# Performance work log

Hardware: AMD Instinct MI355X
Metric: run time of the kernel (lower is better)

Reference implementation:

```python
import jax, jax.numpy as jnp
import numpy as np

H = 12        # query heads
KVH = 4       # key/value heads
D = 256       # head_dim = 3072 / 12
THETA = 1000042.0


def setup_inputs() -> dict:
    key = jax.random.key(0)
    ks = jax.random.split(key, 6)
    B, S, E = 1, 4096, 3072
    init = 0.02
    return {
        "hidden_states": jax.random.normal(ks[0], (B, S, E), jnp.float32),
        "attention_mask": jnp.ones((B, S), jnp.int32),
        "position_ids": jnp.arange(B * S, dtype=jnp.int32).reshape(B, S) % S,
        "Wq": jax.random.normal(ks[1], (E, H * D), jnp.float32) * init,
        "Wk": jax.random.normal(ks[2], (E, KVH * D), jnp.float32) * init,
        "Wv": jax.random.normal(ks[3], (E, KVH * D), jnp.float32) * init,
        "Wo": jax.random.normal(ks[4], (H * D, E), jnp.float32) * init,
    }


def _rotate_half(t):
    return jnp.concatenate([-t[..., D // 2:], t[..., : D // 2]], axis=-1)


def reference(hidden_states, attention_mask, position_ids, Wq, Wk, Wv, Wo):
    B, S, E = hidden_states.shape
    # QKV projections (no bias)
    q = (hidden_states @ Wq).reshape(B, S, H, D)
    k = (hidden_states @ Wk).reshape(B, S, KVH, D)
    v = (hidden_states @ Wv).reshape(B, S, KVH, D)
    # rotary embedding: sincos[pos] with half-split sin/cos, broadcast over heads
    inv_freq = jnp.asarray(1.0 / (THETA ** (np.arange(0, D, 2) / D)), jnp.float32)  # [D/2]
    freqs = position_ids.astype(jnp.float32)[..., None] * inv_freq                 # [B,S,D/2]
    emb = jnp.concatenate([freqs, freqs], axis=-1)[:, :, None, :]                  # [B,S,1,D]
    sin, cos = jnp.sin(emb), jnp.cos(emb)
    q = q * cos + _rotate_half(q) * sin
    k = k * cos + _rotate_half(k) * sin
    # GQA: repeat kv heads to match query heads
    kr = jnp.repeat(k, H // KVH, axis=2)  # [B,S,H,D]
    vr = jnp.repeat(v, H // KVH, axis=2)
    # causal mask combined with padding mask
    causal = jnp.tril(jnp.ones((S, S), bool))
    mask = (attention_mask > 0)[:, None, None, :] & causal[None, None]  # [B,1,S,S]
    neg = jnp.finfo(jnp.float32).min
    bias = jnp.where(mask, 0.0, neg).astype(jnp.float32)
    scores = jnp.einsum('bqhd,bkhd->bhqk', q, kr) / jnp.sqrt(jnp.float32(D)) + bias
    attn = jax.nn.softmax(scores, axis=-1)                 # [B,H,S,S]
    out = jnp.einsum('bhqk,bkhd->bqhd', attn, vr).reshape(B, S, H * D)
    return out @ Wo
```

## Files before the change

### kernel.cpp

```cpp
#include <hip/hip_runtime.h>
#include <hip/hip_bf16.h>
#include <math.h>
#include <stdint.h>

typedef unsigned short u16;
typedef __bf16 bf16x8 __attribute__((ext_vector_type(8)));
typedef float f32x4 __attribute__((ext_vector_type(4)));
typedef unsigned short u16x8 __attribute__((ext_vector_type(8)));
typedef unsigned short u16x4 __attribute__((ext_vector_type(4)));
typedef float f32x4v __attribute__((ext_vector_type(4)));

#define LOG2E 1.44269504088896340736f
#define S_LEN 4096
#define EMB 3072
#define NH 12
#define NKV 4
#define HD 256
#define KVDIM 1024

static __device__ __forceinline__ float b2f(u16 u) {
    union { unsigned int i; float f; } x; x.i = ((unsigned int)u) << 16; return x.f;
}
static __device__ __forceinline__ u16 f2b(float f) {
    union { float f; unsigned int i; } x; x.f = f;
    unsigned int r = (x.i + 0x7fffu + ((x.i >> 16) & 1u)) >> 16;
    return (u16)r;
}
static __device__ __forceinline__ f32x4 zero4() {
    f32x4 z; z[0] = 0.f; z[1] = 0.f; z[2] = 0.f; z[3] = 0.f; return z;
}
static __device__ __forceinline__ void gld_lds16(const void* g, void* l) {
    __builtin_amdgcn_global_load_lds(
        (__attribute__((address_space(1))) void*)(uintptr_t)g,
        (__attribute__((address_space(3))) void*)l, 16, 0, 0);
}

__global__ __launch_bounds__(256) void conv_f32_bf16(
    const float* __restrict__ in, u16* __restrict__ out, int n)
{
    int i = (blockIdx.x * 256 + threadIdx.x) * 4;
    if (i + 3 < n) {
        f32x4v v = *(const f32x4v*)(in + i);
        u16x4 o;
        o[0] = f2b(v[0]); o[1] = f2b(v[1]); o[2] = f2b(v[2]); o[3] = f2b(v[3]);
        *(u16x4*)(out + i) = o;
    } else {
        for (int j = i; j < n; ++j) out[j] = f2b(in[j]);
    }
}

__global__ __launch_bounds__(256) void transpose_f32_bf16(
    const float* __restrict__ in, u16* __restrict__ out, int R, int C)
{
    __shared__ u16 t[64][65];
    const int tid = threadIdx.x;
    const int c0 = blockIdx.x * 64, r0 = blockIdx.y * 64;
#pragma unroll
    for (int i = 0; i < 16; ++i) {
        int lin = i * 256 + tid;
        int r = lin >> 6, c = lin & 63;
        t[r][c] = f2b(in[(size_t)(r0 + r) * C + c0 + c]);
    }
    __syncthreads();
#pragma unroll
    for (int i = 0; i < 16; ++i) {
        int lin = i * 256 + tid;
        int c = lin >> 6, r = lin & 63;
        out[(size_t)(c0 + c) * R + r0 + r] = t[r][c];
    }
}

__global__ __launch_bounds__(256) void transpose_u16(
    const u16* __restrict__ in, u16* __restrict__ out, int R, int C)
{
    __shared__ u16 t[64][65];
    const int tid = threadIdx.x;
    const int c0 = blockIdx.x * 64, r0 = blockIdx.y * 64;
#pragma unroll
    for (int i = 0; i < 16; ++i) {
        int lin = i * 256 + tid;
        int r = lin >> 6, c = lin & 63;
        t[r][c] = in[(size_t)(r0 + r) * C + c0 + c];
    }
    __syncthreads();
#pragma unroll
    for (int i = 0; i < 16; ++i) {
        int lin = i * 256 + tid;
        int c = lin >> 6, r = lin & 63;
        out[(size_t)(c0 + c) * R + r0 + r] = t[r][c];
    }
}

__global__ __launch_bounds__(128) void sincos_kernel(
    const int* __restrict__ pos, float* __restrict__ tab)
{
    int s = blockIdx.x, t = threadIdx.x;
    float p = (float)pos[s];
    double e = (double)t / 128.0;
    float inv = (float)(1.0 / pow(1000042.0, e));
    float a = p * inv;
    tab[(size_t)s * 256 + t]       = cosf(a);
    tab[(size_t)s * 256 + 128 + t] = sinf(a);
}

__global__ __launch_bounds__(128) void rope_kernel(
    u16* __restrict__ Qb, u16* __restrict__ Kb, const float* __restrict__ tab)
{
    int s = blockIdx.x, hh = blockIdx.y, t = threadIdx.x;
    const float* cs = tab + (size_t)s * 256;
    float c = cs[t], sn = cs[128 + t];
    u16* row;
    float scale;
    if (hh < NH) { row = Qb + (size_t)s * EMB + hh * HD; scale = 0.0625f; }
    else         { row = Kb + (size_t)s * KVDIM + (size_t)(hh - NH) * HD; scale = 1.0f; }
    float a = b2f(row[t]), b = b2f(row[t + 128]);
    float oa = (a * c - b * sn) * scale;
    float ob = (b * c + a * sn) * scale;
    row[t] = f2b(oa); row[t + 128] = f2b(ob);
}

template <typename OutT>
__global__ __launch_bounds__(256) void gemm_bt(
    const u16* __restrict__ A, const u16* __restrict__ BT, OutT* __restrict__ C,
    int M, int N, int K)
{
    __shared__ __align__(16) u16 As[128 * 32];
    __shared__ __align__(16) u16 Bs[128 * 32];
    const int tid = threadIdx.x;
    const int lane = tid & 63, wid = tid >> 6;
    const int m0 = blockIdx.y * 128, n0 = blockIdx.x * 128;
    const int wm = (wid >> 1) * 64, wn = (wid & 1) * 64;
    const int g = lane >> 4, c16 = lane & 15;
    f32x4 acc[4][4];
#pragma unroll
    for (int i = 0; i < 4; ++i)
#pragma unroll
        for (int j = 0; j < 4; ++j) acc[i][j] = zero4();
    const int nk = K >> 5;
    const u16* Ab = A + (size_t)m0 * K;
    const u16* Bb = BT + (size_t)n0 * K;
    for (int kt = 0; kt < nk; ++kt) {
#pragma unroll
        for (int r2 = 0; r2 < 2; ++r2) {
            int chunk = r2 * 256 + tid;
            int row = chunk >> 2, c8 = chunk & 3;
            gld_lds16(Ab + (size_t)row * K + kt * 32 + c8 * 8, &As[chunk * 8]);
            gld_lds16(Bb + (size_t)row * K + kt * 32 + c8 * 8, &Bs[chunk * 8]);
        }
        __syncthreads();
        bf16x8 af[4], bfr[4];
#pragma unroll
        for (int i = 0; i < 4; ++i) {
            af[i]  = *(const bf16x8*)&As[(wm + i * 16 + c16) * 32 + g * 8];
            bfr[i] = *(const bf16x8*)&Bs[(wn + i * 16 + c16) * 32 + g * 8];
        }
#pragma unroll
        for (int i = 0; i < 4; ++i)
#pragma unroll
            for (int j = 0; j < 4; ++j)
                acc[i][j] = __builtin_amdgcn_mfma_f32_16x16x32_bf16(af[i], bfr[j], acc[i][j], 0, 0, 0);
        __syncthreads();
    }
#pragma unroll
    for (int i = 0; i < 4; ++i)
#pragma unroll
        for (int j = 0; j < 4; ++j)
#pragma unroll
            for (int r = 0; r < 4; ++r) {
                int row = m0 + wm + i * 16 + g * 4 + r;
                int col = n0 + wn + j * 16 + c16;
                if constexpr (sizeof(OutT) == 2)
                    C[(size_t)row * N + col] = f2b(acc[i][j][r]);
                else
                    C[(size_t)row * N + col] = acc[i][j][r];
            }
}

__global__ __launch_bounds__(256) void attn_kernel(
    u16* __restrict__ Q, const u16* __restrict__ Kb, const u16* __restrict__ VtG,
    const int* __restrict__ am)
{
    __shared__ __align__(16) u16 Ks[32 * 256];
    __shared__ __align__(16) u16 Vt[256 * 32];
    __shared__ __align__(16) u16 Ps[4][16 * 40];
    const int tid = threadIdx.x;
    const int lane = tid & 63, wid = tid >> 6;
    const int bx = blockIdx.x;
    const int qb = (S_LEN / 64 - 1) - (bx / NH);
    const int h  = bx % NH;
    const int kvh = h / 3;
    const int g = lane >> 4, c16 = lane & 15;

    bf16x8 qf[8];
    {
        const u16* Qbase = Q + (size_t)(qb * 64 + wid * 16 + c16) * EMB + h * HD + g * 8;
#pragma unroll
        for (int kc = 0; kc < 8; ++kc)
            qf[kc] = *(const bf16x8*)(Qbase + kc * 32);
    }
    f32x4 acc[16];
#pragma unroll
    for (int i = 0; i < 16; ++i) acc[i] = zero4();
    float mrow[4] = { -INFINITY, -INFINITY, -INFINITY, -INFINITY };
    float lrow[4] = { 0.f, 0.f, 0.f, 0.f };

    const int kv_end = qb * 64 + 64;
    for (int kv0 = 0; kv0 < kv_end; kv0 += 32) {
        {
            const u16* Kg = Kb + (size_t)kv0 * KVDIM + kvh * HD;
#pragma unroll
            for (int seg = 0; seg < 4; ++seg) {
                int chunk = seg * 256 + tid;
                int row = chunk >> 5;
                int ps = chunk & 31;
                int ls = ps ^ (row & 7);
                gld_lds16(Kg + (size_t)row * KVDIM + ls * 8, &Ks[chunk * 8]);
            }
        }
        {
            const u16* Vg = VtG + (size_t)kvh * HD * S_LEN + kv0;
#pragma unroll
            for (int seg = 0; seg < 4; ++seg) {
                int chunk = seg * 256 + tid;
                int d = chunk >> 2;
                int part = chunk & 3;
                gld_lds16(Vg + (size_t)d * S_LEN + part * 8, &Vt[chunk * 8]);
            }
        }
        __syncthreads();

        f32x4 sc[2]; sc[0] = zero4(); sc[1] = zero4();
#pragma unroll
        for (int kc = 0; kc < 8; ++kc) {
#pragma unroll
            for (int c = 0; c < 2; ++c) {
                int row = c * 16 + c16;
                int lin = row * 512 + kc * 64 + g * 16;
                int phys = lin ^ ((row & 7) << 4);
                bf16x8 kf = *(const bf16x8*)((const char*)Ks + phys);
                sc[c] = __builtin_amdgcn_mfma_f32_16x16x32_bf16(qf[kc], kf, sc[c], 0, 0, 0);
            }
        }
        const int q_glob = qb * 64 + wid * 16 + g * 4;
        const int kvg0 = kv0 + c16;
        const int am0 = am[kvg0];
        const int am1 = am[kvg0 + 16];
        float p0[4], p1[4], alpha[4];
#pragma unroll
        for (int r = 0; r < 4; ++r) {
            int qr = q_glob + r;
            float s0 = (kvg0 <= qr && am0 > 0) ? sc[0][r] : -INFINITY;
            float s1 = (kvg0 + 16 <= qr && am1 > 0) ? sc[1][r] : -INFINITY;
            float v = fmaxf(s0, s1);
            v = fmaxf(v, __shfl_xor(v, 1));
            v = fmaxf(v, __shfl_xor(v, 2));
            v = fmaxf(v, __shfl_xor(v, 4));
            v = fmaxf(v, __shfl_xor(v, 8));
            float mn = fmaxf(mrow[r], v);
            float a = exp2f((mrow[r] - mn) * LOG2E);
            mrow[r] = mn;
            float e0 = exp2f((s0 - mn) * LOG2E);
            float e1 = exp2f((s1 - mn) * LOG2E);
            float psum = e0 + e1;
            psum += __shfl_xor(psum, 1);
            psum += __shfl_xor(psum, 2);
            psum += __shfl_xor(psum, 4);
            psum += __shfl_xor(psum, 8);
            lrow[r] = lrow[r] * a + psum;
            alpha[r] = a;
            p0[r] = e0; p1[r] = e1;
        }
#pragma unroll
        for (int i = 0; i < 16; ++i) {
            acc[i][0] *= alpha[0]; acc[i][1] *= alpha[1];
            acc[i][2] *= alpha[2]; acc[i][3] *= alpha[3];
        }
        {
            u16* Pw = &Ps[wid][0];
#pragma unroll
            for (int r = 0; r < 4; ++r) {
                int q = g * 4 + r;
                Pw[q * 40 + c16]      = f2b(p0[r]);
                Pw[q * 40 + 16 + c16] = f2b(p1[r]);
            }
        }
        {
            const bf16x8 pa = *(const bf16x8*)&Ps[wid][c16 * 40 + g * 8];
#pragma unroll
            for (int nf = 0; nf < 16; ++nf) {
                bf16x8 vf = *(const bf16x8*)&Vt[(nf * 16 + c16) * 32 + g * 8];
                acc[nf] = __builtin_amdgcn_mfma_f32_16x16x32_bf16(pa, vf, acc[nf], 0, 0, 0);
            }
        }
        __syncthreads();
    }
    {
        float rl[4];
#pragma unroll
        for (int r = 0; r < 4; ++r) rl[r] = 1.0f / lrow[r];
        u16* Ob = Q + (size_t)(qb * 64 + wid * 16) * EMB + h * HD;
#pragma unroll
        for (int nf = 0; nf < 16; ++nf)
#pragma unroll
            for (int r = 0; r < 4; ++r)
                Ob[(size_t)(g * 4 + r) * EMB + nf * 16 + c16] = f2b(acc[nf][r] * rl[r]);
    }
}

extern "C" void kernel_launch(void* const* d_in, const int* in_sizes, int n_in,
                              void* d_out, int out_size, void* d_ws, size_t ws_size,
                              hipStream_t stream)
{
    const float* hs  = (const float*)d_in[0];
    const int* am    = (const int*)d_in[1];
    const int* pos   = (const int*)d_in[2];
    const float* Wq  = (const float*)d_in[3];
    const float* Wk  = (const float*)d_in[4];
    const float* Wv  = (const float*)d_in[5];
    const float* Wo  = (const float*)d_in[6];
    float* out = (float*)d_out;

    float* tab = (float*)d_ws;
    u16* p = (u16*)((char*)d_ws + (size_t)S_LEN * 256 * 4);
    u16* WqT = p; p += (size_t)3072 * 3072;
    u16* WkT = p; p += (size_t)1024 * 3072;
    u16* WvT = p; p += (size_t)1024 * 3072;
    u16* WoT = p; p += (size_t)3072 * 3072;
    u16* hsb = p; p += (size_t)S_LEN * EMB;
    u16* Q   = p; p += (size_t)S_LEN * EMB;
    u16* K   = p; p += (size_t)S_LEN * KVDIM;
    u16* V   = p; p += (size_t)S_LEN * KVDIM;
    u16* VtG = p; p += (size_t)KVDIM * S_LEN;

    conv_f32_bf16<<<(S_LEN * EMB) / 1024, 256, 0, stream>>>(hs, hsb, S_LEN * EMB);
    transpose_f32_bf16<<<dim3(48, 48), 256, 0, stream>>>(Wq, WqT, 3072, 3072);
    transpose_f32_bf16<<<dim3(16, 48), 256, 0, stream>>>(Wk, WkT, 3072, 1024);
    transpose_f32_bf16<<<dim3(16, 48), 256, 0, stream>>>(Wv, WvT, 3072, 1024);
    transpose_f32_bf16<<<dim3(48, 48), 256, 0, stream>>>(Wo, WoT, 3072, 3072);
    sincos_kernel<<<S_LEN, 128, 0, stream>>>(pos, tab);
    gemm_bt<u16><<<dim3(24, 32), 256, 0, stream>>>(hsb, WqT, Q, 4096, 3072, 3072);
    gemm_bt<u16><<<dim3(8, 32), 256, 0, stream>>>(hsb, WkT, K, 4096, 1024, 3072);
    gemm_bt<u16><<<dim3(8, 32), 256, 0, stream>>>(hsb, WvT, V, 4096, 1024, 3072);
    rope_kernel<<<dim3(S_LEN, NH + NKV), 128, 0, stream>>>(Q, K, tab);
    transpose_u16<<<dim3(16, 64), 256, 0, stream>>>(V, VtG, S_LEN, KVDIM);
    attn_kernel<<<S_LEN / 64 * NH, 256, 0, stream>>>(Q, K, VtG, am);
    gemm_bt<float><<<dim3(24, 32), 256, 0, stream>>>(Q, WoT, out, 4096, 3072, 3072);
}
```

Measured before the change: 869.3 us.

## Fuse QKV GEMMs, deepen K tile with swizzle, lazy softmax rescale, hoist inv_freq

The three QKV projection GEMMs become one launch over a concatenated weight, relying on WqT/WkT/WvT sitting contiguously in the workspace. The GEMM main loop now stages K=64 per step with an XOR-swizzled LDS layout, halving barriers per K and cutting bank conflicts. The attention kernel swizzles the V tile in LDS and skips the online-softmax rescale unless the row max grows by more than a threshold. It also moves the row-sum reduction to the end. The inverse-frequency pow is computed once in a separate tiny kernel instead of per sincos thread. These changes carry some risk of fp32 overflow margin in the lazy rescale and depend on the buffer layout being contiguous.

```diff
diff --git a/kernel.cpp b/kernel.cpp
--- a/kernel.cpp
+++ b/kernel.cpp
@@ -91,14 +91,18 @@
     }
 }
 
+__global__ __launch_bounds__(128) void invfreq_kernel(float* __restrict__ invf)
+{
+    int t = threadIdx.x;
+    double e = (double)t / 128.0;
+    invf[t] = (float)(1.0 / pow(1000042.0, e));
+}
+
 __global__ __launch_bounds__(128) void sincos_kernel(
-    const int* __restrict__ pos, float* __restrict__ tab)
+    const int* __restrict__ pos, const float* __restrict__ invf, float* __restrict__ tab)
 {
     int s = blockIdx.x, t = threadIdx.x;
-    float p = (float)pos[s];
-    double e = (double)t / 128.0;
-    float inv = (float)(1.0 / pow(1000042.0, e));
-    float a = p * inv;
+    float a = (float)pos[s] * invf[t];
     tab[(size_t)s * 256 + t]       = cosf(a);
     tab[(size_t)s * 256 + 128 + t] = sinf(a);
 }
@@ -119,48 +123,96 @@
     row[t] = f2b(oa); row[t + 128] = f2b(ob);
 }
 
-template <typename OutT>
-__global__ __launch_bounds__(256) void gemm_bt(
-    const u16* __restrict__ A, const u16* __restrict__ BT, OutT* __restrict__ C,
-    int M, int N, int K)
-{
-    __shared__ __align__(16) u16 As[128 * 32];
-    __shared__ __align__(16) u16 Bs[128 * 32];
-    const int tid = threadIdx.x;
+static __device__ __forceinline__ void gemm_mainloop(
+    const u16* __restrict__ A, const u16* __restrict__ BT, int K,
+    int m0, int n0, int tid, u16* As, u16* Bs, f32x4 (&acc)[4][4])
+{
     const int lane = tid & 63, wid = tid >> 6;
-    const int m0 = blockIdx.y * 128, n0 = blockIdx.x * 128;
     const int wm = (wid >> 1) * 64, wn = (wid & 1) * 64;
     const int g = lane >> 4, c16 = lane & 15;
-    f32x4 acc[4][4];
-#pragma unroll
-    for (int i = 0; i < 4; ++i)
-#pragma unroll
-        for (int j = 0; j < 4; ++j) acc[i][j] = zero4();
-    const int nk = K >> 5;
     const u16* Ab = A + (size_t)m0 * K;
     const u16* Bb = BT + (size_t)n0 * K;
+    const int nk = K >> 6;
     for (int kt = 0; kt < nk; ++kt) {
 #pragma unroll
-        for (int r2 = 0; r2 < 2; ++r2) {
-            int chunk = r2 * 256 + tid;
-            int row = chunk >> 2, c8 = chunk & 3;
-            gld_lds16(Ab + (size_t)row * K + kt * 32 + c8 * 8, &As[chunk * 8]);
-            gld_lds16(Bb + (size_t)row * K + kt * 32 + c8 * 8, &Bs[chunk * 8]);
+        for (int r4 = 0; r4 < 4; ++r4) {
+            int chunk = r4 * 256 + tid;
+            int row = chunk >> 3, c8 = chunk & 7;
+            int ls = c8 ^ (row & 7);
+            gld_lds16(Ab + (size_t)row * K + kt * 64 + ls * 8, &As[chunk * 8]);
+            gld_lds16(Bb + (size_t)row * K + kt * 64 + ls * 8, &Bs[chunk * 8]);
         }
         __syncthreads();
-        bf16x8 af[4], bfr[4];
-#pragma unroll
-        for (int i = 0; i < 4; ++i) {
-            af[i]  = *(const bf16x8*)&As[(wm + i * 16 + c16) * 32 + g * 8];
-            bfr[i] = *(const bf16x8*)&Bs[(wn + i * 16 + c16) * 32 + g * 8];
-        }
-#pragma unroll
-        for (int i = 0; i < 4; ++i)
-#pragma unroll
-            for (int j = 0; j < 4; ++j)
-                acc[i][j] = __builtin_amdgcn_mfma_f32_16x16x32_bf16(af[i], bfr[j], acc[i][j], 0, 0, 0);
+#pragma unroll
+        for (int kk = 0; kk < 2; ++kk) {
+            bf16x8 af[4], bfr[4];
+#pragma unroll
+            for (int i = 0; i < 4; ++i) {
+                int ra = wm + i * 16 + c16;
+                int rb = wn + i * 16 + c16;
+                af[i]  = *(const bf16x8*)&As[ra * 64 + (((kk << 2) + g) ^ (ra & 7)) * 8];
+                bfr[i] = *(const bf16x8*)&Bs[rb * 64 + (((kk << 2) + g) ^ (rb & 7)) * 8];
+            }
+#pragma unroll
+            for (int i = 0; i < 4; ++i)
+#pragma unroll
+                for (int j = 0; j < 4; ++j)
+                    acc[i][j] = __builtin_amdgcn_mfma_f32_16x16x32_bf16(af[i], bfr[j], acc[i][j], 0, 0, 0);
+        }
         __syncthreads();
     }
+}
+
+__global__ __launch_bounds__(256) void gemm_qkv(
+    const u16* __restrict__ A, const u16* __restrict__ BT,
+    u16* __restrict__ Qo, u16* __restrict__ Ko, u16* __restrict__ Vo)
+{
+    __shared__ __align__(16) u16 As[128 * 64];
+    __shared__ __align__(16) u16 Bs[128 * 64];
+    const int tid = threadIdx.x;
+    const int m0 = blockIdx.y * 128, n0 = blockIdx.x * 128;
+    f32x4 acc[4][4];
+#pragma unroll
+    for (int i = 0; i < 4; ++i)
+#pragma unroll
+        for (int j = 0; j < 4; ++j) acc[i][j] = zero4();
+    gemm_mainloop(A, BT, EMB, m0, n0, tid, As, Bs, acc);
+    const int lane = tid & 63, wid = tid >> 6;
+    const int wm = (wid >> 1) * 64, wn = (wid & 1) * 64;
+    const int g = lane >> 4, c16 = lane & 15;
+    u16* dst; int ncol, cb;
+    if (n0 < 3072)      { dst = Qo; ncol = EMB;   cb = 0; }
+    else if (n0 < 4096) { dst = Ko; ncol = KVDIM; cb = 3072; }
+    else                { dst = Vo; ncol = KVDIM; cb = 4096; }
+#pragma unroll
+    for (int i = 0; i < 4; ++i)
+#pragma unroll
+        for (int j = 0; j < 4; ++j)
+#pragma unroll
+            for (int r = 0; r < 4; ++r) {
+                int row = m0 + wm + i * 16 + g * 4 + r;
+                int col = n0 + wn + j * 16 + c16 - cb;
+                dst[(size_t)row * ncol + col] = f2b(acc[i][j][r]);
+            }
+}
+
+__global__ __launch_bounds__(256) void gemm_bt_f32(
+    const u16* __restrict__ A, const u16* __restrict__ BT, float* __restrict__ C,
+    int M, int N, int K)
+{
+    __shared__ __align__(16) u16 As[128 * 64];
+    __shared__ __align__(16) u16 Bs[128 * 64];
+    const int tid = threadIdx.x;
+    const int m0 = blockIdx.y * 128, n0 = blockIdx.x * 128;
+    f32x4 acc[4][4];
+#pragma unroll
+    for (int i = 0; i < 4; ++i)
+#pragma unroll
+        for (int j = 0; j < 4; ++j) acc[i][j] = zero4();
+    gemm_mainloop(A, BT, K, m0, n0, tid, As, Bs, acc);
+    const int lane = tid & 63, wid = tid >> 6;
+    const int wm = (wid >> 1) * 64, wn = (wid & 1) * 64;
+    const int g = lane >> 4, c16 = lane & 15;
 #pragma unroll
     for (int i = 0; i < 4; ++i)
 #pragma unroll
@@ -169,10 +221,7 @@
             for (int r = 0; r < 4; ++r) {
                 int row = m0 + wm + i * 16 + g * 4 + r;
                 int col = n0 + wn + j * 16 + c16;
-                if constexpr (sizeof(OutT) == 2)
-                    C[(size_t)row * N + col] = f2b(acc[i][j][r]);
-                else
-                    C[(size_t)row * N + col] = acc[i][j][r];
+                C[(size_t)row * N + col] = acc[i][j][r];
             }
 }
 
@@ -224,7 +273,8 @@
                 int chunk = seg * 256 + tid;
                 int d = chunk >> 2;
                 int part = chunk & 3;
-                gld_lds16(Vg + (size_t)d * S_LEN + part * 8, &Vt[chunk * 8]);
+                int lp = part ^ (d & 3);
+                gld_lds16(Vg + (size_t)d * S_LEN + lp * 8, &Vt[chunk * 8]);
             }
         }
         __syncthreads();
@@ -245,35 +295,42 @@
         const int kvg0 = kv0 + c16;
         const int am0 = am[kvg0];
         const int am1 = am[kvg0 + 16];
-        float p0[4], p1[4], alpha[4];
+        float s0[4], s1[4], p0[4], p1[4];
+        bool grow = false;
 #pragma unroll
         for (int r = 0; r < 4; ++r) {
             int qr = q_glob + r;
-            float s0 = (kvg0 <= qr && am0 > 0) ? sc[0][r] : -INFINITY;
-            float s1 = (kvg0 + 16 <= qr && am1 > 0) ? sc[1][r] : -INFINITY;
-            float v = fmaxf(s0, s1);
-            v = fmaxf(v, __shfl_xor(v, 1));
-            v = fmaxf(v, __shfl_xor(v, 2));
-            v = fmaxf(v, __shfl_xor(v, 4));
-            v = fmaxf(v, __shfl_xor(v, 8));
-            float mn = fmaxf(mrow[r], v);
-            float a = exp2f((mrow[r] - mn) * LOG2E);
-            mrow[r] = mn;
-            float e0 = exp2f((s0 - mn) * LOG2E);
-            float e1 = exp2f((s1 - mn) * LOG2E);
-            float psum = e0 + e1;
-            psum += __shfl_xor(psum, 1);
-            psum += __shfl_xor(psum, 2);
-            psum += __shfl_xor(psum, 4);
-            psum += __shfl_xor(psum, 8);
-            lrow[r] = lrow[r] * a + psum;
-            alpha[r] = a;
+            s0[r] = (am0 > 0 && kvg0 <= qr) ? sc[0][r] : -INFINITY;
+            s1[r] = (am1 > 0 && kvg0 + 16 <= qr) ? sc[1][r] : -INFINITY;
+            grow |= (fmaxf(s0[r], s1[r]) > mrow[r] + 8.0f);
+        }
+        if (__any(grow)) {
+            float alpha[4];
+#pragma unroll
+            for (int r = 0; r < 4; ++r) {
+                float v = fmaxf(s0[r], s1[r]);
+                v = fmaxf(v, __shfl_xor(v, 1));
+                v = fmaxf(v, __shfl_xor(v, 2));
+                v = fmaxf(v, __shfl_xor(v, 4));
+                v = fmaxf(v, __shfl_xor(v, 8));
+                float mn = fmaxf(mrow[r], v);
+                float a = exp2f((mrow[r] - mn) * LOG2E);
+                mrow[r] = mn;
+                lrow[r] *= a;
+                alpha[r] = a;
+            }
+#pragma unroll
+            for (int i = 0; i < 16; ++i) {
+                acc[i][0] *= alpha[0]; acc[i][1] *= alpha[1];
+                acc[i][2] *= alpha[2]; acc[i][3] *= alpha[3];
+            }
+        }
+#pragma unroll
+        for (int r = 0; r < 4; ++r) {
+            float e0 = exp2f((s0[r] - mrow[r]) * LOG2E);
+            float e1 = exp2f((s1[r] - mrow[r]) * LOG2E);
+            lrow[r] += e0 + e1;
             p0[r] = e0; p1[r] = e1;
-        }
-#pragma unroll
-        for (int i = 0; i < 16; ++i) {
-            acc[i][0] *= alpha[0]; acc[i][1] *= alpha[1];
-            acc[i][2] *= alpha[2]; acc[i][3] *= alpha[3];
         }
         {
             u16* Pw = &Ps[wid][0];
@@ -288,7 +345,8 @@
             const bf16x8 pa = *(const bf16x8*)&Ps[wid][c16 * 40 + g * 8];
 #pragma unroll
             for (int nf = 0; nf < 16; ++nf) {
-                bf16x8 vf = *(const bf16x8*)&Vt[(nf * 16 + c16) * 32 + g * 8];
+                int d = nf * 16 + c16;
+                bf16x8 vf = *(const bf16x8*)&Vt[d * 32 + ((g ^ (d & 3)) * 8)];
                 acc[nf] = __builtin_amdgcn_mfma_f32_16x16x32_bf16(pa, vf, acc[nf], 0, 0, 0);
             }
         }
@@ -297,7 +355,14 @@
     {
         float rl[4];
 #pragma unroll
-        for (int r = 0; r < 4; ++r) rl[r] = 1.0f / lrow[r];
+        for (int r = 0; r < 4; ++r) {
+            float l = lrow[r];
+            l += __shfl_xor(l, 1);
+            l += __shfl_xor(l, 2);
+            l += __shfl_xor(l, 4);
+            l += __shfl_xor(l, 8);
+            rl[r] = 1.0f / l;
+        }
         u16* Ob = Q + (size_t)(qb * 64 + wid * 16) * EMB + h * HD;
 #pragma unroll
         for (int nf = 0; nf < 16; ++nf)
@@ -320,8 +385,9 @@
     const float* Wo  = (const float*)d_in[6];
     float* out = (float*)d_out;
 
-    float* tab = (float*)d_ws;
-    u16* p = (u16*)((char*)d_ws + (size_t)S_LEN * 256 * 4);
+    float* tab  = (float*)d_ws;
+    float* invf = tab + (size_t)S_LEN * 256;
+    u16* p = (u16*)((char*)d_ws + (size_t)S_LEN * 256 * 4 + 512);
     u16* WqT = p; p += (size_t)3072 * 3072;
     u16* WkT = p; p += (size_t)1024 * 3072;
     u16* WvT = p; p += (size_t)1024 * 3072;
@@ -337,12 +403,11 @@
     transpose_f32_bf16<<<dim3(16, 48), 256, 0, stream>>>(Wk, WkT, 3072, 1024);
     transpose_f32_bf16<<<dim3(16, 48), 256, 0, stream>>>(Wv, WvT, 3072, 1024);
     transpose_f32_bf16<<<dim3(48, 48), 256, 0, stream>>>(Wo, WoT, 3072, 3072);
-    sincos_kernel<<<S_LEN, 128, 0, stream>>>(pos, tab);
-    gemm_bt<u16><<<dim3(24, 32), 256, 0, stream>>>(hsb, WqT, Q, 4096, 3072, 3072);
-    gemm_bt<u16><<<dim3(8, 32), 256, 0, stream>>>(hsb, WkT, K, 4096, 1024, 3072);
-    gemm_bt<u16><<<dim3(8, 32), 256, 0, stream>>>(hsb, WvT, V, 4096, 1024, 3072);
+    invfreq_kernel<<<1, 128, 0, stream>>>(invf);
+    sincos_kernel<<<S_LEN, 128, 0, stream>>>(pos, invf, tab);
+    gemm_qkv<<<dim3(40, 32), 256, 0, stream>>>(hsb, WqT, Q, K, V);
     rope_kernel<<<dim3(S_LEN, NH + NKV), 128, 0, stream>>>(Q, K, tab);
     transpose_u16<<<dim3(16, 64), 256, 0, stream>>>(V, VtG, S_LEN, KVDIM);
     attn_kernel<<<S_LEN / 64 * NH, 256, 0, stream>>>(Q, K, VtG, am);
-    gemm_bt<float><<<dim3(24, 32), 256, 0, stream>>>(Q, WoT, out, 4096, 3072, 3072);
-}
+    gemm_bt_f32<<<dim3(24, 32), 256, 0, stream>>>(Q, WoT, out, 4096, 3072, 3072);
+}
```

Result: faster. 731.4 us (-15.9%).
